# Kernel optimization log

Hardware: AMD Instinct MI355X
Metric: run time of the kernel (lower is better)

The kernel has to match this reference:

```python
import jax, jax.numpy as jnp
import numpy as np
from jax import lax
import math

KS = 7  # attention kernel size
PAD = 3


def conv2d(x, w, b, pad):
    y = lax.conv_general_dilated(x, w, (1, 1), [(pad, pad), (pad, pad)],
                                 dimension_numbers=('NCHW', 'OIHW', 'NCHW'))
    return y + b[None, :, None, None]


def unfold(x):
    # x: [B, C, H, W] -> [B, C, KS*KS, H, W], matching nn.Unfold channel-major order
    B, C, H, W = x.shape
    xp = jnp.pad(x, ((0, 0), (0, 0), (PAD, PAD), (PAD, PAD)))
    patches = [xp[:, :, i:i + H, j:j + W] for i in range(KS) for j in range(KS)]
    return jnp.stack(patches, axis=2)


def setup_inputs() -> dict:
    key = jax.random.key(0)
    ks = jax.random.split(key, 12)
    B, H, W = 1, 256, 256
    s = lambda fan: 1.0 / np.sqrt(fan)
    inp = {
        'x': jax.random.normal(ks[0], (B, 6, H, W), jnp.float32),
        'w0': jax.random.normal(ks[1], (48, 3, 3, 3), jnp.float32) * s(3 * 9),
        'b0': jnp.zeros((48,), jnp.float32),
        'w1': jax.random.normal(ks[2], (48, 48, 3, 3), jnp.float32) * s(48 * 9),
        'b1': jnp.zeros((48,), jnp.float32),
        'w2': jax.random.normal(ks[3], (48, 48, 3, 3), jnp.float32) * s(48 * 9),
        'b2': jnp.zeros((48,), jnp.float32),
        'w3': jax.random.normal(ks[4], (24, 48, 3, 3), jnp.float32) * s(48 * 9),
        'b3': jnp.zeros((24,), jnp.float32),
        'skip_w': jax.random.normal(ks[5], (24, 3, 1, 1), jnp.float32) * s(3),
        'skip_b': jnp.zeros((24,), jnp.float32),
        'q_w': jax.random.normal(ks[6], (24, 24, 1, 1), jnp.float32) * s(24),
        'q_b': jnp.zeros((24,), jnp.float32),
        'k_w': jax.random.normal(ks[7], (24, 24, 1, 1), jnp.float32) * s(24),
        'k_b': jnp.zeros((24,), jnp.float32),
        'v_w': jax.random.normal(ks[8], (24, 24, 1, 1), jnp.float32) * s(24),
        'v_b': jnp.zeros((24,), jnp.float32),
    }
    return inp


def reference(x, w0, b0, w1, b1, w2, b2, w3, b3, skip_w, skip_b,
              q_w, q_b, k_w, k_b, v_w, v_b):
    def submodel(t):
        h = jax.nn.relu(conv2d(t, w0, b0, 1))
        h = jax.nn.relu(conv2d(h, w1, b1, 1))
        h = jax.nn.relu(conv2d(h, w2, b2, 1))
        h = jax.nn.relu(conv2d(h, w3, b3, 1))
        return h + conv2d(t, skip_w, skip_b, 0)

    xa, xb = jnp.split(x, 2, axis=1)  # [B,3,H,W] each
    a = submodel(xa)                  # [B,24,H,W]
    b = submodel(xb)

    Q = conv2d(b, q_w, q_b, 0)        # [B,24,H,W]
    K = unfold(conv2d(a, k_w, k_b, 0))  # [B,24,49,H,W]
    V = unfold(conv2d(a, v_w, v_b, 0))  # [B,24,49,H,W]

    C = Q.shape[1]
    A = jnp.einsum('bchw,bcphw->bphw', Q, K) / math.sqrt(C)
    A = jax.nn.softmax(A, axis=1)     # softmax over 49 local positions
    y = jnp.einsum('bphw,bcphw->bchw', A, V)
    return jnp.concatenate([y + a, b], axis=1)  # [B,48,H,W]
```

## Files before the change

### kernel.cpp

```cpp
#include <hip/hip_runtime.h>
#include <math.h>

#define HH 256
#define WW 256
#define NN (HH * WW)

typedef _Float16 f16;
typedef _Float16 f16x8 __attribute__((ext_vector_type(8)));
typedef _Float16 f16x4 __attribute__((ext_vector_type(4)));
typedef float f32x4 __attribute__((ext_vector_type(4)));

#define OQ 75264

__global__ __launch_bounds__(256) void prep_kernel(
    const float* __restrict__ x, const float* __restrict__ w0,
    const float* __restrict__ w1, const float* __restrict__ w2,
    const float* __restrict__ w3, const float* __restrict__ qw,
    const float* __restrict__ kw, const float* __restrict__ vw,
    f16* __restrict__ xh, f16* __restrict__ bf) {
  if (blockIdx.x < 512) {
    int p = blockIdx.x * 256 + threadIdx.x;
    int z = p >= NN;
    int q = p - z * NN;
    const float* xz = x + (size_t)z * 3 * NN;
    f16x4 v;
    v[0] = (f16)xz[q];
    v[1] = (f16)xz[NN + q];
    v[2] = (f16)xz[2 * NN + q];
    v[3] = (f16)0.f;
    *(f16x4*)(xh + (size_t)p * 4) = v;
    return;
  }
  const int O1 = 1536, O2 = O1 + 27648, O3 = O2 + 27648;
  int e = (blockIdx.x - 512) * 256 + threadIdx.x;
  if (e >= OQ + 3072) return;
  float val = 0.f;
  if (e >= OQ) {
    int idx = e - OQ;
    int mat = idx >> 10;
    int r = idx & 1023;
    int nt = r >> 9;
    int lane = (r >> 3) & 63;
    int j = r & 7;
    int n = lane & 15, quad = lane >> 4;
    int ci = quad * 8 + j, co = nt * 16 + n;
    const float* w = (mat == 0) ? qw : (mat == 1) ? kw : vw;
    if (ci < 24 && co < 24) val = w[co * 24 + ci];
  } else {
    const float* w;
    int COUT, idx, mode;
    if (e < O1)      { w = w0; COUT = 48; idx = e;      mode = 0; }
    else if (e < O2) { w = w1; COUT = 48; idx = e - O1; mode = 1; }
    else if (e < O3) { w = w2; COUT = 48; idx = e - O2; mode = 1; }
    else             { w = w3; COUT = 24; idx = e - O3; mode = 1; }
    int j = idx & 7;
    int lane = (idx >> 3) & 63;
    int rest = idx >> 9;
    int n = lane & 15, quad = lane >> 4;
    if (mode == 0) {
      int nt = rest;
      int k = quad * 8 + j;
      int cout = nt * 16 + n;
      if (k < 27) {
        int tap = k / 3, ci = k - tap * 3;
        val = w[(cout * 3 + ci) * 9 + tap];
      }
    } else {
      int kc = rest & 1;
      int tap = (rest >> 1) % 9;
      int nt = (rest >> 1) / 9;
      int ci = kc * 32 + quad * 8 + j;
      int cout = nt * 16 + n;
      if (ci < 48 && cout < COUT) val = w[(cout * 48 + ci) * 9 + tap];
    }
  }
  bf[e] = (f16)val;
}

__global__ __launch_bounds__(256, 2) void conv0_gemm(
    const f16* __restrict__ xh, const f16* __restrict__ bf0,
    const float* __restrict__ bias, f16* __restrict__ outh) {
  extern __shared__ char smem[];
  const int tid = threadIdx.x;
  const int lane = tid & 63, wave = tid >> 6;
  const int n = lane & 15, quad = lane >> 4;
  const int bx = blockIdx.x * 16, by = blockIdx.y * 16, z = blockIdx.z;
  const f16* xz = xh + (size_t)z * NN * 4;

  {
    int p = tid, y = p >> 4, xcol = p & 15;
    int gy = by + y, gx = bx + xcol;
    f16* row = (f16*)(smem + p * 80);
#pragma unroll
    for (int tap = 0; tap < 9; ++tap) {
      int dy = tap / 3, dx = tap - (tap / 3) * 3;
      int sy = gy + dy - 1, sx = gx + dx - 1;
      f16 c0 = (f16)0.f, c1 = c0, c2 = c0;
      if (sy >= 0 && sy < HH && sx >= 0 && sx < WW) {
        const f16* s = xz + ((size_t)sy * WW + sx) * 4;
        c0 = s[0]; c1 = s[1]; c2 = s[2];
      }
      row[tap * 3 + 0] = c0;
      row[tap * 3 + 1] = c1;
      row[tap * 3 + 2] = c2;
    }
#pragma unroll
    for (int k = 27; k < 32; ++k) row[k] = (f16)0.f;
  }
  __syncthreads();

  f32x4 acc[4][3];
#pragma unroll
  for (int nt = 0; nt < 3; ++nt) {
    float bv = bias[nt * 16 + n];
#pragma unroll
    for (int i = 0; i < 4; ++i) acc[i][nt] = (f32x4){bv, bv, bv, bv};
  }
  f16x8 B[3];
#pragma unroll
  for (int nt = 0; nt < 3; ++nt)
    B[nt] = *(const f16x8*)(bf0 + (nt * 64 + lane) * 8);
#pragma unroll
  for (int i = 0; i < 4; ++i) {
    int r = wave * 4 + i;
    f16x8 a = *(const f16x8*)(smem + (r * 16 + n) * 80 + quad * 16);
#pragma unroll
    for (int nt = 0; nt < 3; ++nt)
      acc[i][nt] =
          __builtin_amdgcn_mfma_f32_16x16x32_f16(a, B[nt], acc[i][nt], 0, 0, 0);
  }

  f16* oz = outh + (size_t)z * NN * 48;
#pragma unroll
  for (int i = 0; i < 4; ++i) {
    int y = by + wave * 4 + i;
#pragma unroll
    for (int nt = 0; nt < 3; ++nt)
#pragma unroll
      for (int reg = 0; reg < 4; ++reg)
        oz[((size_t)y * WW + bx + quad * 4 + reg) * 48 + nt * 16 + n] =
            (f16)fmaxf(acc[i][nt][reg], 0.f);
  }
}

template <int NT, int COUT, bool FUSE>
__global__ __launch_bounds__(256, 2) void gemm_conv(
    const f16* __restrict__ in, const f16* __restrict__ bfr,
    const float* __restrict__ bias, f16* __restrict__ outh,
    const float* __restrict__ xsrc, const float* __restrict__ skw,
    const float* __restrict__ skb) {
  extern __shared__ char smem[];
  float* xt = (float*)(smem + 324 * 144);
  const int tid = threadIdx.x;
  const int lane = tid & 63, wave = tid >> 6;
  const int n = lane & 15, quad = lane >> 4;
  const int bx = blockIdx.x * 16, by = blockIdx.y * 16, z = blockIdx.z;
  const f16* inz = in + (size_t)z * NN * 48;

  for (int p = tid; p < 324; p += 256) {
    int yy = p / 18, xx = p - yy * 18;
    int gy = by + yy - 1, gx = bx + xx - 1;
    float4* dst = (float4*)(smem + p * 144);
    if (gy >= 0 && gy < HH && gx >= 0 && gx < WW) {
      const float4* s = (const float4*)(inz + ((size_t)gy * WW + gx) * 48);
      float4 a0 = s[0], a1 = s[1], a2 = s[2], a3 = s[3], a4 = s[4], a5 = s[5];
      dst[0] = a0; dst[1] = a1; dst[2] = a2;
      dst[3] = a3; dst[4] = a4; dst[5] = a5;
      dst[6] = make_float4(0, 0, 0, 0);
      dst[7] = make_float4(0, 0, 0, 0);
    } else {
      float4 zz = make_float4(0, 0, 0, 0);
#pragma unroll
      for (int c = 0; c < 8; ++c) dst[c] = zz;
    }
  }
  if (FUSE) {
    for (int i = tid; i < 768; i += 256) {
      int c = i >> 8, p = i & 255;
      xt[i] = xsrc[(size_t)z * 3 * NN + c * NN + (by + (p >> 4)) * WW + bx +
                   (p & 15)];
    }
  }
  __syncthreads();

  f32x4 acc[4][NT];
#pragma unroll
  for (int nt = 0; nt < NT; ++nt) {
    int cc = nt * 16 + n;
    float bv = (cc < COUT) ? bias[cc] : 0.f;
#pragma unroll
    for (int i = 0; i < 4; ++i) acc[i][nt] = (f32x4){bv, bv, bv, bv};
  }

  const int r0 = wave * 4;
#pragma unroll
  for (int tap = 0; tap < 9; ++tap) {
    const int dy = tap / 3, dx = tap - dy * 3;
    f16x8 B[2][NT];
#pragma unroll
    for (int kc = 0; kc < 2; ++kc)
#pragma unroll
      for (int nt = 0; nt < NT; ++nt)
        B[kc][nt] =
            *(const f16x8*)(bfr + (((nt * 9 + tap) * 2 + kc) * 64 + lane) * 8);
#pragma unroll
    for (int i = 0; i < 4; ++i) {
      const int p = (r0 + i + dy) * 18 + (n + dx);
      const char* ap = smem + p * 144;
      f16x8 a0 = *(const f16x8*)(ap + quad * 16);
      f16x8 a1 = *(const f16x8*)(ap + 64 + quad * 16);
#pragma unroll
      for (int nt = 0; nt < NT; ++nt)
        acc[i][nt] = __builtin_amdgcn_mfma_f32_16x16x32_f16(a0, B[0][nt],
                                                            acc[i][nt], 0, 0, 0);
#pragma unroll
      for (int nt = 0; nt < NT; ++nt)
        acc[i][nt] = __builtin_amdgcn_mfma_f32_16x16x32_f16(a1, B[1][nt],
                                                            acc[i][nt], 0, 0, 0);
    }
  }

  if (!FUSE) {
    f16* oz = outh + (size_t)z * NN * 48;
#pragma unroll
    for (int i = 0; i < 4; ++i) {
      int y = by + r0 + i;
#pragma unroll
      for (int nt = 0; nt < NT; ++nt)
#pragma unroll
        for (int reg = 0; reg < 4; ++reg)
          oz[((size_t)y * WW + bx + quad * 4 + reg) * 48 + nt * 16 + n] =
              (f16)fmaxf(acc[i][nt][reg], 0.f);
    }
  } else {
    f16* oz = outh + (size_t)z * NN * 32;
#pragma unroll
    for (int i = 0; i < 4; ++i) {
      int y = by + r0 + i;
#pragma unroll
      for (int nt = 0; nt < NT; ++nt) {
        int cc = nt * 16 + n;
        float s0 = 0.f, s1 = 0.f, s2 = 0.f, sb0 = 0.f;
        if (cc < 24) {
          s0 = skw[cc * 3 + 0];
          s1 = skw[cc * 3 + 1];
          s2 = skw[cc * 3 + 2];
          sb0 = skb[cc];
        }
#pragma unroll
        for (int reg = 0; reg < 4; ++reg) {
          float v = 0.f;
          if (cc < 24) {
            int pl = (r0 + i) * 16 + quad * 4 + reg;
            float sk = sb0 + s0 * xt[pl] + s1 * xt[256 + pl] + s2 * xt[512 + pl];
            v = fmaxf(acc[i][nt][reg], 0.f) + sk;
          }
          oz[((size_t)(y * WW + bx + quad * 4 + reg)) * 32 + cc] = (f16)v;
        }
      }
    }
  }
}

__global__ __launch_bounds__(256) void q_mfma(const f16* __restrict__ ABh,
                                              const f16* __restrict__ bf,
                                              const float* __restrict__ qb,
                                              f16* __restrict__ Qh) {
  const int tid = threadIdx.x;
  const int lane = tid & 63, wave = tid >> 6;
  const int n = lane & 15, quad = lane >> 4;
  const f16* src = ABh + (size_t)NN * 32;
  f16x8 QF[2];
#pragma unroll
  for (int nt = 0; nt < 2; ++nt)
    QF[nt] = *(const f16x8*)(bf + OQ + (nt * 64 + lane) * 8);
  float qbias[2];
#pragma unroll
  for (int nt = 0; nt < 2; ++nt) {
    int cc = nt * 16 + n;
    qbias[nt] = (cc < 24) ? qb[cc] : 0.f;
  }
#pragma unroll
  for (int t = 0; t < 4; ++t) {
    int T = blockIdx.x * 16 + wave * 4 + t;
    size_t p0 = (size_t)T * 16;
    f16x8 a8 = *(const f16x8*)(src + p0 * 32 + n * 32 + quad * 8);
#pragma unroll
    for (int nt = 0; nt < 2; ++nt) {
      f32x4 acc = {qbias[nt], qbias[nt], qbias[nt], qbias[nt]};
      acc = __builtin_amdgcn_mfma_f32_16x16x32_f16(a8, QF[nt], acc, 0, 0, 0);
      int cc = nt * 16 + n;
      if (cc < 24) {
#pragma unroll
        for (int reg = 0; reg < 4; ++reg)
          Qh[(p0 + quad * 4 + reg) * 24 + cc] = (f16)acc[reg];
      }
    }
  }
}

__device__ inline float dot8p(f16x8 a, f16x8 b, float acc) {
#if __has_builtin(__builtin_amdgcn_fdot2)
  acc = __builtin_amdgcn_fdot2(__builtin_shufflevector(a, a, 0, 1),
                               __builtin_shufflevector(b, b, 0, 1), acc, false);
  acc = __builtin_amdgcn_fdot2(__builtin_shufflevector(a, a, 2, 3),
                               __builtin_shufflevector(b, b, 2, 3), acc, false);
  acc = __builtin_amdgcn_fdot2(__builtin_shufflevector(a, a, 4, 5),
                               __builtin_shufflevector(b, b, 4, 5), acc, false);
  acc = __builtin_amdgcn_fdot2(__builtin_shufflevector(a, a, 6, 7),
                               __builtin_shufflevector(b, b, 6, 7), acc, false);
  return acc;
#else
#pragma unroll
  for (int i = 0; i < 8; ++i) acc += (float)a[i] * (float)b[i];
  return acc;
#endif
}

__global__ __launch_bounds__(256, 3) void attn_kernel(
    const f16* __restrict__ Qh, const f16* __restrict__ ABh,
    const f16* __restrict__ bf, const float* __restrict__ kb,
    const float* __restrict__ vb, float* __restrict__ out) {
  extern __shared__ f16 kv[];
  const int tid = threadIdx.x;
  const int lane = tid & 63, wave = tid >> 6;
  const int n16 = lane & 15, quad = lane >> 4;
  const int bx = blockIdx.x * 32, by = blockIdx.y * 8;
  const int xl = tid & 31, yl = tid >> 5;
  const int p = (by + yl) * WW + bx + xl;
  const f16* ah = ABh;
  const f16* bh = ABh + (size_t)NN * 32;

  f16x8 q0 = *(const f16x8*)(Qh + (size_t)p * 24);
  f16x8 q1 = *(const f16x8*)(Qh + (size_t)p * 24 + 8);
  f16x8 q2 = *(const f16x8*)(Qh + (size_t)p * 24 + 16);

  for (int idx = tid; idx < 2128; idx += 256) {
    int row = idx / 152;
    int rem = idx - row * 152;
    int pxl = rem >> 2;
    int c = rem & 3;
    int gy = by + row - 3, gx = bx + pxl - 3;
    f16x8 v = {};
    if (gy >= 0 && gy < HH && gx >= 0 && gx < WW)
      v = *(const f16x8*)(ah + ((size_t)(gy * WW + gx)) * 32 + c * 8);
    *(f16x8*)(kv + (row * 38 + pxl) * 56 + c * 8) = v;
  }
  __syncthreads();

  const f16* cs = kv + ((yl + 3) * 38 + xl + 3) * 56;
  f16x8 a0 = *(const f16x8*)(cs);
  f16x8 a1 = *(const f16x8*)(cs + 8);
  f16x8 a2 = *(const f16x8*)(cs + 16);
  __syncthreads();

  {
    f16x8 KF[2], VF[2];
#pragma unroll
    for (int nt = 0; nt < 2; ++nt) {
      KF[nt] = *(const f16x8*)(bf + OQ + 1024 + (nt * 64 + lane) * 8);
      VF[nt] = *(const f16x8*)(bf + OQ + 2048 + (nt * 64 + lane) * 8);
    }
    float kbias[2], vbias[2];
#pragma unroll
    for (int nt = 0; nt < 2; ++nt) {
      int cc = nt * 16 + n16;
      kbias[nt] = (cc < 24) ? kb[cc] : 0.f;
      vbias[nt] = (cc < 24) ? vb[cc] : 0.f;
    }
    for (int t = wave; t < 34; t += 4) {
      f16x8 a8 = *(const f16x8*)(kv + (t * 16 + n16) * 56 + quad * 8);
#pragma unroll
      for (int nt = 0; nt < 2; ++nt) {
        f32x4 ak = {kbias[nt], kbias[nt], kbias[nt], kbias[nt]};
        f32x4 av = {vbias[nt], vbias[nt], vbias[nt], vbias[nt]};
        ak = __builtin_amdgcn_mfma_f32_16x16x32_f16(a8, KF[nt], ak, 0, 0, 0);
        av = __builtin_amdgcn_mfma_f32_16x16x32_f16(a8, VF[nt], av, 0, 0, 0);
        int cc = nt * 16 + n16;
        if (cc < 24) {
#pragma unroll
          for (int reg = 0; reg < 4; ++reg) {
            f16* slot = kv + (t * 16 + quad * 4 + reg) * 56;
            slot[cc] = (f16)ak[reg];
            slot[24 + cc] = (f16)av[reg];
          }
        }
      }
    }
  }
  __syncthreads();

  float s[49];
#pragma unroll
  for (int pp = 0; pp < 49; ++pp) {
    int dy = pp / 7, dx = pp - dy * 7;
    const f16* base = kv + ((yl + dy) * 38 + xl + dx) * 56;
    f16x8 k0 = *(const f16x8*)(base);
    f16x8 k1 = *(const f16x8*)(base + 8);
    f16x8 k2 = *(const f16x8*)(base + 16);
    float d = 0.f;
    d = dot8p(q0, k0, d);
    d = dot8p(q1, k1, d);
    d = dot8p(q2, k2, d);
    s[pp] = d * 0.20412414523193154f;
  }

  float m = s[0];
#pragma unroll
  for (int pp = 1; pp < 49; ++pp) m = fmaxf(m, s[pp]);
  float den = 0.f;
#pragma unroll
  for (int pp = 0; pp < 49; ++pp) {
    float e = __expf(s[pp] - m);
    s[pp] = e;
    den += e;
  }
  const float inv = 1.f / den;

  f16x8 y0 = {}, y1 = {}, y2 = {};
#pragma unroll
  for (int pp = 0; pp < 49; ++pp) {
    int dy = pp / 7, dx = pp - dy * 7;
    const f16* base = kv + ((yl + dy) * 38 + xl + dx) * 56 + 24;
    f16 wh = (f16)(s[pp] * inv);
    f16x8 w8 = {wh, wh, wh, wh, wh, wh, wh, wh};
    f16x8 v0 = *(const f16x8*)(base);
    f16x8 v1 = *(const f16x8*)(base + 8);
    f16x8 v2 = *(const f16x8*)(base + 16);
    y0 = v0 * w8 + y0;
    y1 = v1 * w8 + y1;
    y2 = v2 * w8 + y2;
  }

  f16x8 b0 = *(const f16x8*)(bh + (size_t)p * 32);
  f16x8 b1 = *(const f16x8*)(bh + (size_t)p * 32 + 8);
  f16x8 b2 = *(const f16x8*)(bh + (size_t)p * 32 + 16);
#pragma unroll
  for (int c = 0; c < 8; ++c) {
    out[(size_t)c * NN + p] = (float)y0[c] + (float)a0[c];
    out[(size_t)(8 + c) * NN + p] = (float)y1[c] + (float)a1[c];
    out[(size_t)(16 + c) * NN + p] = (float)y2[c] + (float)a2[c];
    out[(size_t)(24 + c) * NN + p] = (float)b0[c];
    out[(size_t)(32 + c) * NN + p] = (float)b1[c];
    out[(size_t)(40 + c) * NN + p] = (float)b2[c];
  }
}

extern "C" void kernel_launch(void* const* d_in, const int* in_sizes, int n_in,
                              void* d_out, int out_size, void* d_ws,
                              size_t ws_size, hipStream_t stream) {
  const float* x = (const float*)d_in[0];
  const float* w0 = (const float*)d_in[1];
  const float* b0 = (const float*)d_in[2];
  const float* w1 = (const float*)d_in[3];
  const float* b1 = (const float*)d_in[4];
  const float* w2 = (const float*)d_in[5];
  const float* b2 = (const float*)d_in[6];
  const float* w3 = (const float*)d_in[7];
  const float* b3 = (const float*)d_in[8];
  const float* sw = (const float*)d_in[9];
  const float* sb = (const float*)d_in[10];
  const float* qw = (const float*)d_in[11];
  const float* qb = (const float*)d_in[12];
  const float* kw = (const float*)d_in[13];
  const float* kb = (const float*)d_in[14];
  const float* vw = (const float*)d_in[15];
  const float* vb = (const float*)d_in[16];
  float* out = (float*)d_out;
  float* ws = (float*)d_ws;

  f16* Qh = (f16*)(ws);
  f16* ABh = (f16*)(ws + (size_t)12 * NN);
  f16* ACT0 = (f16*)(ws + (size_t)44 * NN);
  f16* ACT1 = (f16*)(ws + (size_t)92 * NN);
  f16* XH = (f16*)(ws + (size_t)140 * NN);
  f16* BF = (f16*)(ws + (size_t)144 * NN);

  prep_kernel<<<dim3(818), dim3(256), 0, stream>>>(x, w0, w1, w2, w3, qw, kw,
                                                   vw, XH, BF);

  dim3 cgrd(16, 16, 2);
  conv0_gemm<<<cgrd, dim3(256), 256 * 80, stream>>>(XH, BF, b0, ACT0);
  gemm_conv<3, 48, false><<<cgrd, dim3(256), 324 * 144, stream>>>(
      ACT0, BF + 1536, b1, ACT1, nullptr, nullptr, nullptr);
  gemm_conv<3, 48, false><<<cgrd, dim3(256), 324 * 144, stream>>>(
      ACT1, BF + 29184, b2, ACT0, nullptr, nullptr, nullptr);
  gemm_conv<2, 24, true><<<cgrd, dim3(256), 324 * 144 + 3072, stream>>>(
      ACT0, BF + 56832, b3, ABh, x, sw, sb);

  q_mfma<<<dim3(256), dim3(256), 0, stream>>>(ABh, BF, qb, Qh);

  attn_kernel<<<dim3(8, 32), dim3(256), 544 * 112, stream>>>(Qh, ABh, BF, kb,
                                                             vb, out);
}
```

Baseline: 155.4 us.

## Halve conv tile height, raise occupancy, reorder weight fragment layout

```diff
diff --git a/kernel.cpp b/kernel.cpp
--- a/kernel.cpp
+++ b/kernel.cpp
@@ -46,33 +46,36 @@
     int ci = quad * 8 + j, co = nt * 16 + n;
     const float* w = (mat == 0) ? qw : (mat == 1) ? kw : vw;
     if (ci < 24 && co < 24) val = w[co * 24 + ci];
+  } else if (e < O1) {
+    int idx = e;
+    int j = idx & 7;
+    int lane = (idx >> 3) & 63;
+    int nt = idx >> 9;
+    int n = lane & 15, quad = lane >> 4;
+    int k = quad * 8 + j;
+    int cout = nt * 16 + n;
+    if (k < 27) {
+      int tap = k / 3, ci = k - tap * 3;
+      val = w0[(cout * 3 + ci) * 9 + tap];
+    }
   } else {
     const float* w;
-    int COUT, idx, mode;
-    if (e < O1)      { w = w0; COUT = 48; idx = e;      mode = 0; }
-    else if (e < O2) { w = w1; COUT = 48; idx = e - O1; mode = 1; }
-    else if (e < O3) { w = w2; COUT = 48; idx = e - O2; mode = 1; }
-    else             { w = w3; COUT = 24; idx = e - O3; mode = 1; }
+    int COUT, idx;
+    if (e < O2)      { w = w1; COUT = 48; idx = e - O1; }
+    else if (e < O3) { w = w2; COUT = 48; idx = e - O2; }
+    else             { w = w3; COUT = 24; idx = e - O3; }
+    const int NT = (COUT == 48) ? 3 : 2;
     int j = idx & 7;
     int lane = (idx >> 3) & 63;
     int rest = idx >> 9;
+    int nt = rest % NT;
+    int q2 = rest / NT;
+    int kc = q2 & 1;
+    int tap = q2 >> 1;
     int n = lane & 15, quad = lane >> 4;
-    if (mode == 0) {
-      int nt = rest;
-      int k = quad * 8 + j;
-      int cout = nt * 16 + n;
-      if (k < 27) {
-        int tap = k / 3, ci = k - tap * 3;
-        val = w[(cout * 3 + ci) * 9 + tap];
-      }
-    } else {
-      int kc = rest & 1;
-      int tap = (rest >> 1) % 9;
-      int nt = (rest >> 1) / 9;
-      int ci = kc * 32 + quad * 8 + j;
-      int cout = nt * 16 + n;
-      if (ci < 48 && cout < COUT) val = w[(cout * 48 + ci) * 9 + tap];
-    }
+    int ci = kc * 32 + quad * 8 + j;
+    int cout = nt * 16 + n;
+    if (ci < 48 && cout < COUT) val = w[(cout * 48 + ci) * 9 + tap];
   }
   bf[e] = (f16)val;
 }
@@ -144,20 +147,21 @@
 }
 
 template <int NT, int COUT, bool FUSE>
-__global__ __launch_bounds__(256, 2) void gemm_conv(
+__global__ __launch_bounds__(256, 4) void gemm_conv(
     const f16* __restrict__ in, const f16* __restrict__ bfr,
     const float* __restrict__ bias, f16* __restrict__ outh,
     const float* __restrict__ xsrc, const float* __restrict__ skw,
     const float* __restrict__ skb) {
   extern __shared__ char smem[];
-  float* xt = (float*)(smem + 324 * 144);
+  float* xt = (float*)(smem + 180 * 144);
   const int tid = threadIdx.x;
   const int lane = tid & 63, wave = tid >> 6;
   const int n = lane & 15, quad = lane >> 4;
-  const int bx = blockIdx.x * 16, by = blockIdx.y * 16, z = blockIdx.z;
+  const int bx = blockIdx.x * 16, by = blockIdx.y * 8, z = blockIdx.z;
   const f16* inz = in + (size_t)z * NN * 48;
 
-  for (int p = tid; p < 324; p += 256) {
+  if (tid < 180) {
+    int p = tid;
     int yy = p / 18, xx = p - yy * 18;
     int gy = by + yy - 1, gx = bx + xx - 1;
     float4* dst = (float4*)(smem + p * 144);
@@ -175,25 +179,25 @@
     }
   }
   if (FUSE) {
-    for (int i = tid; i < 768; i += 256) {
-      int c = i >> 8, p = i & 255;
+    for (int i = tid; i < 384; i += 256) {
+      int c = i >> 7, p = i & 127;
       xt[i] = xsrc[(size_t)z * 3 * NN + c * NN + (by + (p >> 4)) * WW + bx +
                    (p & 15)];
     }
   }
   __syncthreads();
 
-  f32x4 acc[4][NT];
+  f32x4 acc[2][NT];
 #pragma unroll
   for (int nt = 0; nt < NT; ++nt) {
     int cc = nt * 16 + n;
     float bv = (cc < COUT) ? bias[cc] : 0.f;
 #pragma unroll
-    for (int i = 0; i < 4; ++i) acc[i][nt] = (f32x4){bv, bv, bv, bv};
-  }
-
-  const int r0 = wave * 4;
-#pragma unroll
+    for (int i = 0; i < 2; ++i) acc[i][nt] = (f32x4){bv, bv, bv, bv};
+  }
+
+  const int r0 = wave * 2;
+#pragma unroll 1
   for (int tap = 0; tap < 9; ++tap) {
     const int dy = tap / 3, dx = tap - dy * 3;
     f16x8 B[2][NT];
@@ -201,10 +205,10 @@
     for (int kc = 0; kc < 2; ++kc)
 #pragma unroll
       for (int nt = 0; nt < NT; ++nt)
-        B[kc][nt] =
-            *(const f16x8*)(bfr + (((nt * 9 + tap) * 2 + kc) * 64 + lane) * 8);
-#pragma unroll
-    for (int i = 0; i < 4; ++i) {
+        B[kc][nt] = *(const f16x8*)(bfr +
+                                    (((tap * 2 + kc) * NT + nt) * 64 + lane) * 8);
+#pragma unroll
+    for (int i = 0; i < 2; ++i) {
       const int p = (r0 + i + dy) * 18 + (n + dx);
       const char* ap = smem + p * 144;
       f16x8 a0 = *(const f16x8*)(ap + quad * 16);
@@ -223,7 +227,7 @@
   if (!FUSE) {
     f16* oz = outh + (size_t)z * NN * 48;
 #pragma unroll
-    for (int i = 0; i < 4; ++i) {
+    for (int i = 0; i < 2; ++i) {
       int y = by + r0 + i;
 #pragma unroll
       for (int nt = 0; nt < NT; ++nt)
@@ -235,7 +239,7 @@
   } else {
     f16* oz = outh + (size_t)z * NN * 32;
 #pragma unroll
-    for (int i = 0; i < 4; ++i) {
+    for (int i = 0; i < 2; ++i) {
       int y = by + r0 + i;
 #pragma unroll
       for (int nt = 0; nt < NT; ++nt) {
@@ -252,7 +256,7 @@
           float v = 0.f;
           if (cc < 24) {
             int pl = (r0 + i) * 16 + quad * 4 + reg;
-            float sk = sb0 + s0 * xt[pl] + s1 * xt[256 + pl] + s2 * xt[512 + pl];
+            float sk = sb0 + s0 * xt[pl] + s1 * xt[128 + pl] + s2 * xt[256 + pl];
             v = fmaxf(acc[i][nt][reg], 0.f) + sk;
           }
           oz[((size_t)(y * WW + bx + quad * 4 + reg)) * 32 + cc] = (f16)v;
@@ -479,13 +483,14 @@
   prep_kernel<<<dim3(818), dim3(256), 0, stream>>>(x, w0, w1, w2, w3, qw, kw,
                                                    vw, XH, BF);
 
-  dim3 cgrd(16, 16, 2);
-  conv0_gemm<<<cgrd, dim3(256), 256 * 80, stream>>>(XH, BF, b0, ACT0);
-  gemm_conv<3, 48, false><<<cgrd, dim3(256), 324 * 144, stream>>>(
+  conv0_gemm<<<dim3(16, 16, 2), dim3(256), 256 * 80, stream>>>(XH, BF, b0,
+                                                               ACT0);
+  dim3 g2(16, 32, 2);
+  gemm_conv<3, 48, false><<<g2, dim3(256), 180 * 144, stream>>>(
       ACT0, BF + 1536, b1, ACT1, nullptr, nullptr, nullptr);
-  gemm_conv<3, 48, false><<<cgrd, dim3(256), 324 * 144, stream>>>(
+  gemm_conv<3, 48, false><<<g2, dim3(256), 180 * 144, stream>>>(
       ACT1, BF + 29184, b2, ACT0, nullptr, nullptr, nullptr);
-  gemm_conv<2, 24, true><<<cgrd, dim3(256), 324 * 144 + 3072, stream>>>(
+  gemm_conv<2, 24, true><<<g2, dim3(256), 180 * 144 + 1536, stream>>>(
       ACT0, BF + 56832, b3, ABh, x, sw, sb);
 
   q_mfma<<<dim3(256), dim3(256), 0, stream>>>(ABh, BF, qb, Qh);
```

Result: slower. 158.8 us (+2.2%).
